# Kernel tuning notes

Hardware: AMD Instinct MI355X
Metric: run time of the kernel (lower is better)

## Reference

```python
import jax, jax.numpy as jnp
import numpy as np

EPS = 1e-6  # annotated-transformer LayerNorm eps


def setup_inputs() -> dict:
    key = jax.random.key(0)
    ks = jax.random.split(key, 6)
    B, S, D, F, G_dom = 32, 512, 1024, 2048, 4
    x = jax.random.normal(ks[0], (B, S, D), dtype=jnp.float32)
    # disjoint partition of the batch into 4 equal domain groups (like the
    # per-domain LongTensor index lists in the torch forward)
    perm = jax.random.permutation(ks[1], B).astype(jnp.int32)
    idx = perm.reshape(G_dom, B // G_dom)  # [4, 8]
    s1 = 1.0 / np.sqrt(D)
    s2 = 1.0 / np.sqrt(F)
    W1 = jax.random.normal(ks[2], (G_dom, D, F), dtype=jnp.float32) * s1
    B1 = jnp.zeros((G_dom, F), dtype=jnp.float32)
    W2 = jax.random.normal(ks[3], (G_dom, F, D), dtype=jnp.float32) * s2
    B2 = jnp.zeros((G_dom, D), dtype=jnp.float32)
    G = jnp.ones((G_dom, D), dtype=jnp.float32)
    Bn = jnp.zeros((G_dom, D), dtype=jnp.float32)
    return {"x": x, "idx": idx, "W1": W1, "B1": B1, "W2": W2, "B2": B2,
            "G": G, "Bn": Bn}


def _layer_norm(x, g, b):
    # matches torch: a_2 * (x - mean) / (std + eps) + b_2, std unbiased (ddof=1)
    mu = jnp.mean(x, axis=-1, keepdims=True)
    sd = jnp.std(x, axis=-1, keepdims=True, ddof=1)
    return g * (x - mu) / (sd + EPS) + b


def reference(x, idx, W1, B1, W2, B2, G, Bn):
    # gather per-domain token groups: [n_dom, per_dom, S, D]
    xg = x[idx]
    # SublayerConnection (eval mode, dropout off): x + adapter(norm(x))
    h = _layer_norm(xg, G[:, None, None, :], Bn[:, None, None, :])
    h = jax.nn.relu(jnp.einsum('gbsd,gdf->gbsf', h, W1) + B1[:, None, None, :])
    a = jnp.einsum('gbsf,gfd->gbsd', h, W2) + B2[:, None, None, :]
    out_g = xg + a
    # scatter combine (index_copy): indices are a disjoint partition
    S_, D_ = x.shape[1], x.shape[2]
    out = jnp.zeros_like(x).at[idx.reshape(-1)].set(out_g.reshape(-1, S_, D_))
    return out
```

## Files before the change

### kernel.cpp

```cpp
#include <hip/hip_runtime.h>
#include <hip/hip_bf16.h>


#define S_DIM 512
#define D_DIM 1024
#define F_DIM 2048
#define MPG   4096

typedef __attribute__((ext_vector_type(8))) short  short8;
typedef __attribute__((ext_vector_type(4))) float  f32x4;

__device__ __forceinline__ void gll16(const void* g, void* l) {
  __builtin_amdgcn_global_load_lds((__attribute__((address_space(1))) void*)g,
                                   (__attribute__((address_space(3))) void*)l,
                                   16, 0, 0);
}
#define VMC4()  asm volatile("s_waitcnt vmcnt(4)" ::: "memory")
#define BAR()   __builtin_amdgcn_s_barrier()

__global__ __launch_bounds__(256) void transpose_cast_kernel(
    const float* __restrict__ W1, const float* __restrict__ W2,
    __hip_bfloat16* __restrict__ W1t, __hip_bfloat16* __restrict__ W2t)
{
  __shared__ float tl[32][33];
  const int bid = blockIdx.x;
  const float* src; __hip_bfloat16* dst;
  int R, C, tr, tc;
  if (bid < 8192) {
    const int g = bid >> 11, t = bid & 2047;
    R = 1024; C = 2048; tr = t >> 6; tc = t & 63;
    src = W1 + (size_t)g * R * C;
    dst = W1t + (size_t)g * R * C;
  } else {
    const int b2 = bid - 8192;
    const int g = b2 >> 11, t = b2 & 2047;
    R = 2048; C = 1024; tr = t >> 5; tc = t & 31;
    src = W2 + (size_t)g * R * C;
    dst = W2t + (size_t)g * R * C;
  }
  const int tx = threadIdx.x & 31, ty = threadIdx.x >> 5;
  const int r0 = tr * 32, c0 = tc * 32;
#pragma unroll
  for (int i = 0; i < 4; ++i)
    tl[ty + 8 * i][tx] = src[(size_t)(r0 + ty + 8 * i) * C + (c0 + tx)];
  __syncthreads();
#pragma unroll
  for (int i = 0; i < 4; ++i)
    dst[(size_t)(c0 + ty + 8 * i) * R + (r0 + tx)] = __float2bfloat16(tl[tx][ty + 8 * i]);
}

__global__ __launch_bounds__(256) void ln_gather_kernel(
    const float* __restrict__ x, const int* __restrict__ idx,
    const float* __restrict__ G, const float* __restrict__ Bn,
    __hip_bfloat16* __restrict__ Xn)
{
  const int wid  = (blockIdx.x * 256 + threadIdx.x) >> 6;
  const int lane = threadIdx.x & 63;
  const int g = wid >> 12;
  const int r = wid & 4095;
  const int j = r >> 9;
  const int tok = r & 511;
  const int b = idx[g * 8 + j];

  const float* src = x + ((size_t)b * S_DIM + tok) * D_DIM + lane * 16;
  float4 vq[4];
#pragma unroll
  for (int i = 0; i < 4; ++i) vq[i] = ((const float4*)src)[i];
  const float* va = (const float*)vq;

  float s = 0.f, s2 = 0.f;
#pragma unroll
  for (int i = 0; i < 16; ++i) { s += va[i]; s2 += va[i] * va[i]; }
#pragma unroll
  for (int o = 32; o > 0; o >>= 1) { s += __shfl_xor(s, o); s2 += __shfl_xor(s2, o); }

  const float mu  = s * (1.0f / 1024.0f);
  float var = fmaxf(s2 * (1.0f / 1024.0f) - mu * mu, 0.0f) * (1024.0f / 1023.0f);
  const float rs  = 1.0f / (sqrtf(var) + 1e-6f);

  float4 gq[4], bq[4];
  const float* gp = G  + (size_t)g * D_DIM + lane * 16;
  const float* bp = Bn + (size_t)g * D_DIM + lane * 16;
#pragma unroll
  for (int i = 0; i < 4; ++i) { gq[i] = ((const float4*)gp)[i]; bq[i] = ((const float4*)bp)[i]; }
  const float* ga = (const float*)gq;
  const float* be = (const float*)bq;

  __align__(16) __hip_bfloat16 ob[16];
#pragma unroll
  for (int i = 0; i < 16; ++i)
    ob[i] = __float2bfloat16(ga[i] * (va[i] - mu) * rs + be[i]);

  __hip_bfloat16* dst = Xn + ((size_t)g * MPG + r) * D_DIM + lane * 16;
  ((uint4*)dst)[0] = *(const uint4*)&ob[0];
  ((uint4*)dst)[1] = *(const uint4*)&ob[8];
}

template <bool SECOND>
__global__ __launch_bounds__(512, 2) void gemm_kernel(
    const __hip_bfloat16* __restrict__ A,
    const __hip_bfloat16* __restrict__ Bw,
    const float* __restrict__ bias,
    const float* __restrict__ xres,
    const int* __restrict__ idx,
    __hip_bfloat16* __restrict__ obf,
    float* __restrict__ of32,
    const int N, const int K, const int NT)
{
  extern __shared__ char lds[];
  const int ntile = N >> 8;
  const int nwg = gridDim.x;
  const int bid0 = blockIdx.x;
  const int bid = (bid0 & 7) * (nwg >> 3) + (bid0 >> 3);
  const int mt = bid / ntile, nt = bid % ntile;
  const int g  = mt >> 4;
  const int tid = threadIdx.x;
  const int w = tid >> 6, lane = tid & 63;
  const int wm = w >> 2, wn = w & 3;

  const __hip_bfloat16* Ab = A + (size_t)mt * 256 * K;
  const __hip_bfloat16* Bb = Bw + ((size_t)g * N + (size_t)nt * 256) * K;

  const int sp   = (lane & 7) ^ ((lane >> 3) & 7);
  const int srow = 2 * (lane >> 3) + (sp >> 2);
  const int skof = (sp & 3) * 8;
  const __hip_bfloat16* Ag0 = Ab + (size_t)(w * 32 + srow) * K + skof;
  const __hip_bfloat16* Ag1 = Ag0 + (size_t)16 * K;
  const __hip_bfloat16* Bg0 = Bb + (size_t)(w * 32 + srow) * K + skof;
  const __hip_bfloat16* Bg1 = Bg0 + (size_t)16 * K;

  const int l15 = lane & 15, sl = lane >> 4;
  const int slot_phys = (((l15 & 1) << 2) + sl) ^ ((l15 >> 1) & 7);
  const int lane_c = ((l15 >> 1) << 7) + (slot_phys << 4);

  f32x4 acc[8][4] = {};
  short8 frA[4], frB[4];

#define STAGE(BUFX, MAT, KH, TN) {                                          \
    const int koff = (TN) * 64 + (KH) * 32;                                 \
    char* d = lds + (BUFX) + ((KH) * 2 + (MAT)) * 16384 + w * 2048;         \
    if (MAT) { gll16(Bg0 + koff, d); gll16(Bg1 + koff, d + 1024); }         \
    else     { gll16(Ag0 + koff, d); gll16(Ag1 + koff, d + 1024); } }

#define RDA(BUFX, KH, MH) {                                                 \
    const char* base_ = lds + (BUFX) + (KH) * 32768 + wm * 8192 +           \
                        (MH) * 4096 + lane_c;                               \
    _Pragma("unroll") for (int mm = 0; mm < 4; ++mm)                        \
      frA[mm] = *(const short8*)(base_ + mm * 1024); }

#define RDB(BUFX, KH) {                                                     \
    const char* base_ = lds + (BUFX) + 16384 + (KH) * 32768 + wn * 4096 +   \
                        lane_c;                                             \
    _Pragma("unroll") for (int n = 0; n < 4; ++n)                           \
      frB[n] = *(const short8*)(base_ + n * 1024); }

#define MF(MH) {                                                            \
    __builtin_amdgcn_s_setprio(1);                                          \
    _Pragma("unroll") for (int mm = 0; mm < 4; ++mm)                        \
      _Pragma("unroll") for (int n = 0; n < 4; ++n)                         \
        acc[(MH) * 4 + mm][n] = __builtin_amdgcn_mfma_f32_16x16x32_bf16(    \
            frA[mm], frB[n], acc[(MH) * 4 + mm][n], 0, 0, 0);               \
    __builtin_amdgcn_s_setprio(0); }

  STAGE(0, 0, 0, 0); STAGE(0, 1, 0, 0); STAGE(0, 0, 1, 0); STAGE(0, 1, 1, 0);

  for (int t = 0; t < NT; ++t) {
    const int bufb = (t & 1) << 16;
    const int bufx = bufb ^ 65536;
    const int more = (t + 1 < NT);
    const int tn = more ? t + 1 : 0;
    VMC4();
    BAR();
    RDB(bufb, 0); RDA(bufb, 0, 0);
    if (more) STAGE(bufx, 0, 0, tn);
    MF(0);
    BAR();
    RDA(bufb, 0, 1);
    if (more) STAGE(bufx, 1, 0, tn);
    MF(1);
    VMC4();
    BAR();
    RDB(bufb, 1); RDA(bufb, 1, 0);
    if (more) STAGE(bufx, 0, 1, tn);
    MF(0);
    BAR();
    RDA(bufb, 1, 1);
    if (more) STAGE(bufx, 1, 1, tn);
    MF(1);
  }
#undef STAGE
#undef RDA
#undef RDB
#undef MF

  const int cc  = lane & 15;
  const int cr4 = (lane >> 4) * 4;

  float bv[4];
#pragma unroll
  for (int n = 0; n < 4; ++n)
    bv[n] = bias[(size_t)g * N + nt * 256 + wn * 64 + n * 16 + cc];

  float* wsl = (float*)(lds + w * 4352);
  const int rr  = lane >> 3;
  const int c8  = (lane & 7) * 8;
  const int gcol0 = nt * 256 + wn * 64 + c8;

  if constexpr (!SECOND) {
#pragma unroll
    for (int p = 0; p < 8; ++p) {
#pragma unroll
      for (int n = 0; n < 4; ++n)
#pragma unroll
        for (int i = 0; i < 4; ++i)
          wsl[(cr4 + i) * 68 + n * 16 + cc] = fmaxf(acc[p][n][i] + bv[n], 0.0f);
      const int grow0 = mt * 256 + wm * 128 + p * 16;
#pragma unroll
      for (int it = 0; it < 2; ++it) {
        const int r = it * 8 + rr;
        float4 v0 = *(const float4*)&wsl[r * 68 + c8];
        float4 v1 = *(const float4*)&wsl[r * 68 + c8 + 4];
        __align__(16) __hip_bfloat16 ob[8];
        ob[0] = __float2bfloat16(v0.x); ob[1] = __float2bfloat16(v0.y);
        ob[2] = __float2bfloat16(v0.z); ob[3] = __float2bfloat16(v0.w);
        ob[4] = __float2bfloat16(v1.x); ob[5] = __float2bfloat16(v1.y);
        ob[6] = __float2bfloat16(v1.z); ob[7] = __float2bfloat16(v1.w);
        *(uint4*)&obf[(size_t)(grow0 + r) * N + gcol0] = *(const uint4*)ob;
      }
    }
  } else {
    const int rbase = (mt & 15) * 256;
    const int b = idx[g * 8 + (rbase >> 9)];
    const size_t ob = (size_t)b * S_DIM * D_DIM;
#pragma unroll
    for (int p = 0; p < 8; ++p) {
#pragma unroll
      for (int n = 0; n < 4; ++n)
#pragma unroll
        for (int i = 0; i < 4; ++i)
          wsl[(cr4 + i) * 68 + n * 16 + cc] = acc[p][n][i] + bv[n];
      const int rloc0 = rbase + wm * 128 + p * 16;
#pragma unroll
      for (int it = 0; it < 2; ++it) {
        const int r = it * 8 + rr;
        const int tok = (rloc0 + r) & 511;
        const size_t off = ob + (size_t)tok * D_DIM + gcol0;
        float4 v0 = *(const float4*)&wsl[r * 68 + c8];
        float4 v1 = *(const float4*)&wsl[r * 68 + c8 + 4];
        float4 x0 = *(const float4*)&xres[off];
        float4 x1 = *(const float4*)&xres[off + 4];
        v0.x += x0.x; v0.y += x0.y; v0.z += x0.z; v0.w += x0.w;
        v1.x += x1.x; v1.y += x1.y; v1.z += x1.z; v1.w += x1.w;
        *(float4*)&of32[off]     = v0;
        *(float4*)&of32[off + 4] = v1;
      }
    }
  }
}

extern "C" void kernel_launch(void* const* d_in, const int* in_sizes, int n_in,
                              void* d_out, int out_size, void* d_ws, size_t ws_size,
                              hipStream_t stream) {
  const float* x  = (const float*)d_in[0];
  const int*   idx = (const int*)d_in[1];
  const float* W1 = (const float*)d_in[2];
  const float* B1 = (const float*)d_in[3];
  const float* W2 = (const float*)d_in[4];
  const float* B2 = (const float*)d_in[5];
  const float* G  = (const float*)d_in[6];
  const float* Bn = (const float*)d_in[7];
  float* out = (float*)d_out;

  char* ws = (char*)d_ws;
  __hip_bfloat16* Xn  = (__hip_bfloat16*)(ws);
  __hip_bfloat16* W1t = (__hip_bfloat16*)(ws + 33554432);
  __hip_bfloat16* W2t = (__hip_bfloat16*)(ws + 50331648);
  __hip_bfloat16* H1  = (__hip_bfloat16*)(ws + 67108864);

  (void)hipFuncSetAttribute((const void*)gemm_kernel<false>,
                            hipFuncAttributeMaxDynamicSharedMemorySize, 131072);
  (void)hipFuncSetAttribute((const void*)gemm_kernel<true>,
                            hipFuncAttributeMaxDynamicSharedMemorySize, 131072);

  transpose_cast_kernel<<<dim3(16384), dim3(256), 0, stream>>>(W1, W2, W1t, W2t);
  ln_gather_kernel<<<dim3(4096), dim3(256), 0, stream>>>(x, idx, G, Bn, Xn);
  gemm_kernel<false><<<dim3(512), dim3(512), 131072, stream>>>(
      Xn, W1t, B1, nullptr, nullptr, H1, nullptr, F_DIM, D_DIM, 16);
  gemm_kernel<true><<<dim3(256), dim3(512), 131072, stream>>>(
      H1, W2t, B2, x, idx, nullptr, out, D_DIM, F_DIM, 32);
}
```

Measured before the change: 183.9 us.

## Merge prep kernels and restructure GEMM K-loop to one barrier per tile

Folds the weight transpose/cast and the layernorm-gather into a single launch with block-range dispatch, removing one kernel launch. The GEMM main loop now issues all eight global-to-LDS loads for the next K tile at once, waits with vmcnt(0) and a single barrier per tile, and reads both K halves into doubled fragment registers before the MFMAs. This cuts barrier count and aims at a simpler schedule. In exchange it raises register pressure and gives up the finer-grained overlap of partial-tile waits, and the next tile's loads now start only after the first half of the MFMAs.

```diff
diff --git a/kernel.cpp b/kernel.cpp
--- a/kernel.cpp
+++ b/kernel.cpp
@@ -15,46 +15,47 @@
                                    (__attribute__((address_space(3))) void*)l,
                                    16, 0, 0);
 }
-#define VMC4()  asm volatile("s_waitcnt vmcnt(4)" ::: "memory")
+#define VMC0()  asm volatile("s_waitcnt vmcnt(0)" ::: "memory")
+#define SB()    __builtin_amdgcn_sched_barrier(0)
 #define BAR()   __builtin_amdgcn_s_barrier()
 
-__global__ __launch_bounds__(256) void transpose_cast_kernel(
+__global__ __launch_bounds__(256) void prep_kernel(
     const float* __restrict__ W1, const float* __restrict__ W2,
-    __hip_bfloat16* __restrict__ W1t, __hip_bfloat16* __restrict__ W2t)
+    const float* __restrict__ x,  const int* __restrict__ idx,
+    const float* __restrict__ G,  const float* __restrict__ Bn,
+    __hip_bfloat16* __restrict__ W1t, __hip_bfloat16* __restrict__ W2t,
+    __hip_bfloat16* __restrict__ Xn)
 {
   __shared__ float tl[32][33];
   const int bid = blockIdx.x;
-  const float* src; __hip_bfloat16* dst;
-  int R, C, tr, tc;
-  if (bid < 8192) {
-    const int g = bid >> 11, t = bid & 2047;
-    R = 1024; C = 2048; tr = t >> 6; tc = t & 63;
-    src = W1 + (size_t)g * R * C;
-    dst = W1t + (size_t)g * R * C;
-  } else {
-    const int b2 = bid - 8192;
-    const int g = b2 >> 11, t = b2 & 2047;
-    R = 2048; C = 1024; tr = t >> 5; tc = t & 31;
-    src = W2 + (size_t)g * R * C;
-    dst = W2t + (size_t)g * R * C;
+  if (bid < 16384) {
+    const float* src; __hip_bfloat16* dst;
+    int R, C, tr, tc;
+    if (bid < 8192) {
+      const int g = bid >> 11, t = bid & 2047;
+      R = 1024; C = 2048; tr = t >> 6; tc = t & 63;
+      src = W1 + (size_t)g * R * C;
+      dst = W1t + (size_t)g * R * C;
+    } else {
+      const int b2 = bid - 8192;
+      const int g = b2 >> 11, t = b2 & 2047;
+      R = 2048; C = 1024; tr = t >> 5; tc = t & 31;
+      src = W2 + (size_t)g * R * C;
+      dst = W2t + (size_t)g * R * C;
+    }
+    const int tx = threadIdx.x & 31, ty = threadIdx.x >> 5;
+    const int r0 = tr * 32, c0 = tc * 32;
+#pragma unroll
+    for (int i = 0; i < 4; ++i)
+      tl[ty + 8 * i][tx] = src[(size_t)(r0 + ty + 8 * i) * C + (c0 + tx)];
+    __syncthreads();
+#pragma unroll
+    for (int i = 0; i < 4; ++i)
+      dst[(size_t)(c0 + ty + 8 * i) * R + (r0 + tx)] = __float2bfloat16(tl[tx][ty + 8 * i]);
+    return;
   }
-  const int tx = threadIdx.x & 31, ty = threadIdx.x >> 5;
-  const int r0 = tr * 32, c0 = tc * 32;
-#pragma unroll
-  for (int i = 0; i < 4; ++i)
-    tl[ty + 8 * i][tx] = src[(size_t)(r0 + ty + 8 * i) * C + (c0 + tx)];
-  __syncthreads();
-#pragma unroll
-  for (int i = 0; i < 4; ++i)
-    dst[(size_t)(c0 + ty + 8 * i) * R + (r0 + tx)] = __float2bfloat16(tl[tx][ty + 8 * i]);
-}
-
-__global__ __launch_bounds__(256) void ln_gather_kernel(
-    const float* __restrict__ x, const int* __restrict__ idx,
-    const float* __restrict__ G, const float* __restrict__ Bn,
-    __hip_bfloat16* __restrict__ Xn)
-{
-  const int wid  = (blockIdx.x * 256 + threadIdx.x) >> 6;
+  const int lb   = bid - 16384;
+  const int wid  = lb * 4 + (threadIdx.x >> 6);
   const int lane = threadIdx.x & 63;
   const int g = wid >> 12;
   const int r = wid & 4095;
@@ -134,64 +135,58 @@
   const int lane_c = ((l15 >> 1) << 7) + (slot_phys << 4);
 
   f32x4 acc[8][4] = {};
-  short8 frA[4], frB[4];
-
-#define STAGE(BUFX, MAT, KH, TN) {                                          \
-    const int koff = (TN) * 64 + (KH) * 32;                                 \
-    char* d = lds + (BUFX) + ((KH) * 2 + (MAT)) * 16384 + w * 2048;         \
-    if (MAT) { gll16(Bg0 + koff, d); gll16(Bg1 + koff, d + 1024); }         \
-    else     { gll16(Ag0 + koff, d); gll16(Ag1 + koff, d + 1024); } }
-
-#define RDA(BUFX, KH, MH) {                                                 \
-    const char* base_ = lds + (BUFX) + (KH) * 32768 + wm * 8192 +           \
-                        (MH) * 4096 + lane_c;                               \
-    _Pragma("unroll") for (int mm = 0; mm < 4; ++mm)                        \
-      frA[mm] = *(const short8*)(base_ + mm * 1024); }
-
-#define RDB(BUFX, KH) {                                                     \
-    const char* base_ = lds + (BUFX) + 16384 + (KH) * 32768 + wn * 4096 +   \
-                        lane_c;                                             \
-    _Pragma("unroll") for (int n = 0; n < 4; ++n)                           \
-      frB[n] = *(const short8*)(base_ + n * 1024); }
-
-#define MF(MH) {                                                            \
+  short8 frA[2][4], frB[2][4];
+
+#define STAGE4(BUFX, TN) {                                                  \
+    const int k0 = (TN) * 64;                                               \
+    char* d0 = lds + (BUFX) + w * 2048;                                     \
+    gll16(Ag0 + k0,      d0);         gll16(Ag1 + k0,      d0 + 1024);      \
+    gll16(Bg0 + k0,      d0 + 16384); gll16(Bg1 + k0,      d0 + 17408);     \
+    gll16(Ag0 + k0 + 32, d0 + 32768); gll16(Ag1 + k0 + 32, d0 + 33792);     \
+    gll16(Bg0 + k0 + 32, d0 + 49152); gll16(Bg1 + k0 + 32, d0 + 50176); }
+
+#define RDA2(BUFB, MH) {                                                    \
+    _Pragma("unroll") for (int kh = 0; kh < 2; ++kh) {                      \
+      const char* b_ = lds + (BUFB) + kh * 32768 + wm * 8192 +              \
+                       (MH) * 4096 + lane_c;                                \
+      _Pragma("unroll") for (int mm = 0; mm < 4; ++mm)                      \
+        frA[kh][mm] = *(const short8*)(b_ + mm * 1024); } }
+
+#define RDB2(BUFB) {                                                        \
+    _Pragma("unroll") for (int kh = 0; kh < 2; ++kh) {                      \
+      const char* b_ = lds + (BUFB) + 16384 + kh * 32768 + wn * 4096 +      \
+                       lane_c;                                              \
+      _Pragma("unroll") for (int n = 0; n < 4; ++n)                         \
+        frB[kh][n] = *(const short8*)(b_ + n * 1024); } }
+
+#define MF32(MH) {                                                          \
     __builtin_amdgcn_s_setprio(1);                                          \
-    _Pragma("unroll") for (int mm = 0; mm < 4; ++mm)                        \
-      _Pragma("unroll") for (int n = 0; n < 4; ++n)                         \
-        acc[(MH) * 4 + mm][n] = __builtin_amdgcn_mfma_f32_16x16x32_bf16(    \
-            frA[mm], frB[n], acc[(MH) * 4 + mm][n], 0, 0, 0);               \
+    _Pragma("unroll") for (int kh = 0; kh < 2; ++kh)                        \
+      _Pragma("unroll") for (int mm = 0; mm < 4; ++mm)                      \
+        _Pragma("unroll") for (int n = 0; n < 4; ++n)                       \
+          acc[(MH) * 4 + mm][n] = __builtin_amdgcn_mfma_f32_16x16x32_bf16(  \
+              frA[kh][mm], frB[kh][n], acc[(MH) * 4 + mm][n], 0, 0, 0);     \
     __builtin_amdgcn_s_setprio(0); }
 
-  STAGE(0, 0, 0, 0); STAGE(0, 1, 0, 0); STAGE(0, 0, 1, 0); STAGE(0, 1, 1, 0);
+  STAGE4(0, 0);
 
   for (int t = 0; t < NT; ++t) {
     const int bufb = (t & 1) << 16;
     const int bufx = bufb ^ 65536;
-    const int more = (t + 1 < NT);
-    const int tn = more ? t + 1 : 0;
-    VMC4();
+    VMC0();
     BAR();
-    RDB(bufb, 0); RDA(bufb, 0, 0);
-    if (more) STAGE(bufx, 0, 0, tn);
-    MF(0);
-    BAR();
-    RDA(bufb, 0, 1);
-    if (more) STAGE(bufx, 1, 0, tn);
-    MF(1);
-    VMC4();
-    BAR();
-    RDB(bufb, 1); RDA(bufb, 1, 0);
-    if (more) STAGE(bufx, 0, 1, tn);
-    MF(0);
-    BAR();
-    RDA(bufb, 1, 1);
-    if (more) STAGE(bufx, 1, 1, tn);
-    MF(1);
+    SB();
+    RDB2(bufb);
+    RDA2(bufb, 0);
+    MF32(0);
+    if (t + 1 < NT) STAGE4(bufx, t + 1);
+    RDA2(bufb, 1);
+    MF32(1);
   }
-#undef STAGE
-#undef RDA
-#undef RDB
-#undef MF
+#undef STAGE4
+#undef RDA2
+#undef RDB2
+#undef MF32
 
   const int cc  = lane & 15;
   const int cr4 = (lane >> 4) * 4;
@@ -282,8 +277,8 @@
   (void)hipFuncSetAttribute((const void*)gemm_kernel<true>,
                             hipFuncAttributeMaxDynamicSharedMemorySize, 131072);
 
-  transpose_cast_kernel<<<dim3(16384), dim3(256), 0, stream>>>(W1, W2, W1t, W2t);
-  ln_gather_kernel<<<dim3(4096), dim3(256), 0, stream>>>(x, idx, G, Bn, Xn);
+  prep_kernel<<<dim3(20480), dim3(256), 0, stream>>>(
+      W1, W2, x, idx, G, Bn, W1t, W2t, Xn);
   gemm_kernel<false><<<dim3(512), dim3(512), 131072, stream>>>(
       Xn, W1t, B1, nullptr, nullptr, H1, nullptr, F_DIM, D_DIM, 16);
   gemm_kernel<true><<<dim3(256), dim3(512), 131072, stream>>>(
```

New measurement: 171.3 us, median of 2. -6.8%, faster.
